# Optimization experiments

Hardware: AMD Instinct MI355X
Metric: run time of the kernel (lower is better)

The kernel has to match this reference:

```python
import jax, jax.numpy as jnp
import numpy as np

NUM_HEADS = 16


def setup_inputs() -> dict:
    key = jax.random.key(0)
    k1, k2, k3 = jax.random.split(key, 3)
    B, S, E = 2, 2048, 1024
    hidden_states = jax.random.normal(k1, (B, S, E), dtype=jnp.float32)
    c_attn_w = jax.random.normal(k2, (E, 3 * E), dtype=jnp.float32) * 0.02
    c_attn_b = jnp.zeros((3 * E,), dtype=jnp.float32)
    c_proj_w = jax.random.normal(k3, (E, E), dtype=jnp.float32) * 0.02
    c_proj_b = jnp.zeros((E,), dtype=jnp.float32)
    return {
        "hidden_states": hidden_states,
        "c_attn_w": c_attn_w,
        "c_attn_b": c_attn_b,
        "c_proj_w": c_proj_w,
        "c_proj_b": c_proj_b,
    }


def reference(hidden_states, c_attn_w, c_attn_b, c_proj_w, c_proj_b):
    B, S, E = hidden_states.shape
    H = NUM_HEADS
    D = E // H
    # Conv1D: qkv projection -> [B, S, 3E]
    qkv = jnp.einsum("bse,ef->bsf", hidden_states, c_attn_w) + c_attn_b
    q, k, v = jnp.split(qkv, 3, axis=-1)
    # split heads -> [B, H, S, D]
    def heads(x):
        return x.reshape(B, S, H, D).transpose(0, 2, 1, 3)
    q, k, v = heads(q), heads(k), heads(v)
    # scaled QK^T -> [B, H, S, S]
    scale = jnp.asarray(D, dtype=q.dtype) ** 0.5
    attn_weights = jnp.einsum("bhqd,bhkd->bhqk", q, k) / scale
    # causal mask (bias buffer): True on/below diagonal
    causal = jnp.tril(jnp.ones((S, S), dtype=bool))
    mask_value = jnp.finfo(attn_weights.dtype).min
    attn_weights = jnp.where(causal[None, None, :, :], attn_weights, mask_value)
    attn_weights = jax.nn.softmax(attn_weights, axis=-1)
    # attn @ V -> merge heads -> [B, S, E]
    attn_out = jnp.einsum("bhqk,bhkd->bhqd", attn_weights, v)
    attn_out = attn_out.transpose(0, 2, 1, 3).reshape(B, S, E)
    # output projection (Conv1D)
    out = jnp.einsum("bse,ef->bsf", attn_out, c_proj_w) + c_proj_b
    return out
```

## Files before the change

kernel.cpp:

```cpp
#include <hip/hip_runtime.h>
#include <stdint.h>

typedef __attribute__((ext_vector_type(8))) __bf16 bf16x8;
typedef __attribute__((ext_vector_type(4))) __bf16 bf16x4;
typedef __attribute__((ext_vector_type(4))) float f32x4;

#define MFMA16(a, b, c) __builtin_amdgcn_mfma_f32_16x16x32_bf16(a, b, c, 0, 0, 0)

__global__ __launch_bounds__(256) void k_cast_bf16(const float* __restrict__ in,
                                                   __bf16* __restrict__ out, int n) {
    int i = (blockIdx.x * 256 + threadIdx.x) * 4;
    if (i >= n) return;
    float4 v = *(const float4*)(in + i);
    bf16x4 o;
    o.x = (__bf16)v.x; o.y = (__bf16)v.y; o.z = (__bf16)v.z; o.w = (__bf16)v.w;
    *(bf16x4*)(out + i) = o;
}

__global__ __launch_bounds__(256) void k_transpose_cast(const float* __restrict__ in,
                                                        __bf16* __restrict__ out,
                                                        int R, int C) {
    __shared__ __bf16 tile[32][33];
    int c0 = blockIdx.x * 32, r0 = blockIdx.y * 32;
    int tx = threadIdx.x, ty = threadIdx.y;
#pragma unroll
    for (int i = 0; i < 4; i++)
        tile[ty + i * 8][tx] = (__bf16)in[(size_t)(r0 + ty + i * 8) * C + c0 + tx];
    __syncthreads();
#pragma unroll
    for (int i = 0; i < 4; i++)
        out[(size_t)(c0 + ty + i * 8) * R + r0 + tx] = tile[tx][ty + i * 8];
}

__global__ __launch_bounds__(256, 2) void k_gemm_qkv(
    const __bf16* __restrict__ A, const __bf16* __restrict__ Bt,
    const float* __restrict__ bias,
    __bf16* __restrict__ Qo, __bf16* __restrict__ Ko, __bf16* __restrict__ Vo) {
    __shared__ __bf16 As[128 * 40];
    __shared__ __bf16 Bs[128 * 40];
    const int Kd = 1024;
    int n0 = blockIdx.x * 128, m0 = blockIdx.y * 128;
    int tid = threadIdx.x;
    int wv = tid >> 6, lane = tid & 63;
    int wm = (wv >> 1) * 64, wn = (wv & 1) * 64;
    int quad = lane >> 4, l16 = lane & 15;
    f32x4 acc[4][4] = {};
    for (int k0 = 0; k0 < Kd; k0 += 32) {
        __syncthreads();
#pragma unroll
        for (int it = 0; it < 2; it++) {
            int c = tid + it * 256;
            int row = c >> 2, kc = (c & 3) << 3;
            *(uint4*)(&As[row * 40 + kc]) = *(const uint4*)(&A[(size_t)(m0 + row) * Kd + k0 + kc]);
            *(uint4*)(&Bs[row * 40 + kc]) = *(const uint4*)(&Bt[(size_t)(n0 + row) * Kd + k0 + kc]);
        }
        __syncthreads();
        bf16x8 af[4], bfr[4];
#pragma unroll
        for (int i = 0; i < 4; i++)
            af[i] = *(const bf16x8*)(&As[(wm + i * 16 + l16) * 40 + quad * 8]);
#pragma unroll
        for (int j = 0; j < 4; j++)
            bfr[j] = *(const bf16x8*)(&Bs[(wn + j * 16 + l16) * 40 + quad * 8]);
#pragma unroll
        for (int i = 0; i < 4; i++)
#pragma unroll
            for (int j = 0; j < 4; j++)
                acc[i][j] = MFMA16(af[i], bfr[j], acc[i][j]);
    }
#pragma unroll
    for (int i = 0; i < 4; i++) {
#pragma unroll
        for (int j = 0; j < 4; j++) {
            int n = n0 + wn + j * 16 + l16;
            float bv = bias[n];
            int sec = n >> 10, nl = n & 1023;
            int h = nl >> 6, d = nl & 63;
            int mbase = m0 + wm + i * 16 + quad * 4;
            int bb = mbase >> 11, s = mbase & 2047;
            if (sec == 2) {
                bf16x4 v4;
#pragma unroll
                for (int r = 0; r < 4; r++) v4[r] = (__bf16)(acc[i][j][r] + bv);
                *(bf16x4*)(&Vo[((size_t)(bb * 16 + h) * 64 + d) * 2048 + s]) = v4;
            } else {
                __bf16* dst = sec == 0 ? Qo : Ko;
                float scl = (sec == 0) ? 0.125f : 1.0f;
#pragma unroll
                for (int r = 0; r < 4; r++)
                    dst[((size_t)(bb * 16 + h) * 2048 + (s + r)) * 64 + d] =
                        (__bf16)((acc[i][j][r] + bv) * scl);
            }
        }
    }
}

__global__ __launch_bounds__(256, 2) void k_gemm_proj(
    const __bf16* __restrict__ A, const __bf16* __restrict__ Bt,
    const float* __restrict__ bias, float* __restrict__ out) {
    __shared__ __bf16 As[128 * 40];
    __shared__ __bf16 Bs[128 * 40];
    const int Kd = 1024;
    int n0 = blockIdx.x * 128, m0 = blockIdx.y * 128;
    int tid = threadIdx.x;
    int wv = tid >> 6, lane = tid & 63;
    int wm = (wv >> 1) * 64, wn = (wv & 1) * 64;
    int quad = lane >> 4, l16 = lane & 15;
    f32x4 acc[4][4] = {};
    for (int k0 = 0; k0 < Kd; k0 += 32) {
        __syncthreads();
#pragma unroll
        for (int it = 0; it < 2; it++) {
            int c = tid + it * 256;
            int row = c >> 2, kc = (c & 3) << 3;
            *(uint4*)(&As[row * 40 + kc]) = *(const uint4*)(&A[(size_t)(m0 + row) * Kd + k0 + kc]);
            *(uint4*)(&Bs[row * 40 + kc]) = *(const uint4*)(&Bt[(size_t)(n0 + row) * Kd + k0 + kc]);
        }
        __syncthreads();
        bf16x8 af[4], bfr[4];
#pragma unroll
        for (int i = 0; i < 4; i++)
            af[i] = *(const bf16x8*)(&As[(wm + i * 16 + l16) * 40 + quad * 8]);
#pragma unroll
        for (int j = 0; j < 4; j++)
            bfr[j] = *(const bf16x8*)(&Bs[(wn + j * 16 + l16) * 40 + quad * 8]);
#pragma unroll
        for (int i = 0; i < 4; i++)
#pragma unroll
            for (int j = 0; j < 4; j++)
                acc[i][j] = MFMA16(af[i], bfr[j], acc[i][j]);
    }
#pragma unroll
    for (int i = 0; i < 4; i++) {
#pragma unroll
        for (int j = 0; j < 4; j++) {
            int n = n0 + wn + j * 16 + l16;
            float bv = bias[n];
#pragma unroll
            for (int r = 0; r < 4; r++) {
                int m = m0 + wm + i * 16 + quad * 4 + r;
                out[(size_t)m * 1024 + n] = acc[i][j][r] + bv;
            }
        }
    }
}

__global__ __launch_bounds__(256, 2) void k_attn(
    const __bf16* __restrict__ Qg, const __bf16* __restrict__ Kg,
    const __bf16* __restrict__ Vtg, __bf16* __restrict__ Og) {
    __shared__ __bf16 Ks[64 * 72];
    __shared__ __bf16 Vt[64 * 72];
    __shared__ __bf16 Ps[64 * 72];
    int bh = blockIdx.x >> 4;
    int tp = blockIdx.x & 15;
    int b = bh >> 4, h = bh & 15;
    const __bf16* Qp = Qg + (size_t)bh * 2048 * 64;
    const __bf16* Kp = Kg + (size_t)bh * 2048 * 64;
    const __bf16* Vp = Vtg + (size_t)bh * 64 * 2048;
    int tid = threadIdx.x, wv = tid >> 6, lane = tid & 63;
    int quad = lane >> 4, l16 = lane & 15;
    int tt0 = tp, tt1 = 31 - tp;

    bf16x8 qf[2][2];
#pragma unroll
    for (int ks = 0; ks < 2; ks++) {
        qf[0][ks] = *(const bf16x8*)(&Qp[(size_t)(tt0 * 64 + wv * 16 + l16) * 64 + ks * 32 + quad * 8]);
        qf[1][ks] = *(const bf16x8*)(&Qp[(size_t)(tt1 * 64 + wv * 16 + l16) * 64 + ks * 32 + quad * 8]);
    }
    float m_i[2] = {-1e30f, -1e30f}, l_i[2] = {0.f, 0.f};
    f32x4 acc_o[2][4] = {};

    int nkt = tt1 + 1;
    for (int kt = 0; kt < nkt; kt++) {
        __syncthreads();
#pragma unroll
        for (int it = 0; it < 2; it++) {
            int idx = tid * 2 + it;
            int row = idx >> 3, cc = (idx & 7) * 8;
            *(uint4*)(&Ks[row * 72 + cc]) =
                *(const uint4*)(&Kp[(size_t)(kt * 64 + row) * 64 + cc]);
            *(uint4*)(&Vt[row * 72 + cc]) =
                *(const uint4*)(&Vp[(size_t)row * 2048 + kt * 64 + cc]);
        }
        __syncthreads();
        bf16x8 kf[4][2], vf[4][2];
#pragma unroll
        for (int i = 0; i < 4; i++)
#pragma unroll
            for (int ks = 0; ks < 2; ks++) {
                kf[i][ks] = *(const bf16x8*)(&Ks[(i * 16 + l16) * 72 + ks * 32 + quad * 8]);
                vf[i][ks] = *(const bf16x8*)(&Vt[(i * 16 + l16) * 72 + ks * 32 + quad * 8]);
            }
#pragma unroll
        for (int tt = 0; tt < 2; tt++) {
            int t = tt ? tt1 : tt0;
            if (kt > t) continue;
            f32x4 s[4] = {};
#pragma unroll
            for (int ks = 0; ks < 2; ks++)
#pragma unroll
                for (int i = 0; i < 4; i++) s[i] = MFMA16(kf[i][ks], qf[tt][ks], s[i]);
            if (kt == t) {
                int ql = wv * 16 + l16;
#pragma unroll
                for (int i = 0; i < 4; i++)
#pragma unroll
                    for (int r = 0; r < 4; r++)
                        if (i * 16 + quad * 4 + r > ql) s[i][r] = -1e30f;
            }
            float mx = s[0][0];
#pragma unroll
            for (int i = 0; i < 4; i++)
#pragma unroll
                for (int r = 0; r < 4; r++) mx = fmaxf(mx, s[i][r]);
            mx = fmaxf(mx, __shfl_xor(mx, 16));
            mx = fmaxf(mx, __shfl_xor(mx, 32));
            float mnew = fmaxf(m_i[tt], mx);
            float al = __expf(m_i[tt] - mnew);
            m_i[tt] = mnew;
            float rs = 0.f;
#pragma unroll
            for (int i = 0; i < 4; i++) {
                bf16x4 pk;
#pragma unroll
                for (int r = 0; r < 4; r++) {
                    float p = __expf(s[i][r] - mnew);
                    rs += p;
                    pk[r] = (__bf16)p;
                }
                *(bf16x4*)(&Ps[(wv * 16 + l16) * 72 + i * 16 + quad * 4]) = pk;
            }
            rs += __shfl_xor(rs, 16);
            rs += __shfl_xor(rs, 32);
            l_i[tt] = l_i[tt] * al + rs;
#pragma unroll
            for (int i = 0; i < 4; i++)
#pragma unroll
                for (int r = 0; r < 4; r++) acc_o[tt][i][r] *= al;
#pragma unroll
            for (int ks = 0; ks < 2; ks++) {
                bf16x8 pf = *(const bf16x8*)(&Ps[(wv * 16 + l16) * 72 + ks * 32 + quad * 8]);
#pragma unroll
                for (int i = 0; i < 4; i++) acc_o[tt][i] = MFMA16(vf[i][ks], pf, acc_o[tt][i]);
            }
        }
    }
#pragma unroll
    for (int tt = 0; tt < 2; tt++) {
        int t = tt ? tt1 : tt0;
        int q = t * 64 + wv * 16 + l16;
        float inv = 1.f / l_i[tt];
#pragma unroll
        for (int i = 0; i < 4; i++) {
            bf16x4 o4;
#pragma unroll
            for (int r = 0; r < 4; r++) o4[r] = (__bf16)(acc_o[tt][i][r] * inv);
            *(bf16x4*)(&Og[((size_t)b * 2048 + q) * 1024 + h * 64 + i * 16 + quad * 4]) = o4;
        }
    }
}

extern "C" void kernel_launch(void* const* d_in, const int* in_sizes, int n_in,
                              void* d_out, int out_size, void* d_ws, size_t ws_size,
                              hipStream_t stream) {
    const float* hs = (const float*)d_in[0];
    const float* w1 = (const float*)d_in[1];
    const float* b1 = (const float*)d_in[2];
    const float* w2 = (const float*)d_in[3];
    const float* b2 = (const float*)d_in[4];
    float* out = (float*)d_out;

    char* ws = (char*)d_ws;
    __bf16* hsb = (__bf16*)(ws);
    __bf16* w1t = (__bf16*)(ws + (size_t)8 * 1024 * 1024);
    __bf16* w2t = (__bf16*)(ws + (size_t)14 * 1024 * 1024);
    __bf16* Qb  = (__bf16*)(ws + (size_t)16 * 1024 * 1024);
    __bf16* Kb  = (__bf16*)(ws + (size_t)24 * 1024 * 1024);
    __bf16* Vb  = (__bf16*)(ws + (size_t)32 * 1024 * 1024);
    __bf16* AOb = (__bf16*)(ws + (size_t)40 * 1024 * 1024);

    k_cast_bf16<<<4096, 256, 0, stream>>>(hs, hsb, 4096 * 1024);
    k_transpose_cast<<<dim3(96, 32), dim3(32, 8), 0, stream>>>(w1, w1t, 1024, 3072);
    k_transpose_cast<<<dim3(32, 32), dim3(32, 8), 0, stream>>>(w2, w2t, 1024, 1024);
    k_gemm_qkv<<<dim3(24, 32), 256, 0, stream>>>(hsb, w1t, b1, Qb, Kb, Vb);
    k_attn<<<512, 256, 0, stream>>>(Qb, Kb, Vb, AOb);
    k_gemm_proj<<<dim3(8, 32), 256, 0, stream>>>(AOb, w2t, b2, out);
}
```

Measured before the change: 199.5 us.

## Use direct global-to-LDS loads in GEMMs and one query tile per attention block

Both GEMM kernels now load A and B tiles with global_load_lds, which writes directly into unpadded LDS. This skips the register staging round trip but drops the bank-conflict padding. The attention kernel drops the paired-tile scheme and processes one query tile per block, launching twice as many blocks with heaviest tiles scheduled first. That lowers per-block register state and improves parallelism, at the cost of possible load imbalance and more K/V reloads.

```diff
diff --git a/kernel.cpp b/kernel.cpp
--- a/kernel.cpp
+++ b/kernel.cpp
@@ -6,6 +6,12 @@
 typedef __attribute__((ext_vector_type(4))) float f32x4;
 
 #define MFMA16(a, b, c) __builtin_amdgcn_mfma_f32_16x16x32_bf16(a, b, c, 0, 0, 0)
+
+__device__ __forceinline__ void async_ld16(const __bf16* g, __bf16* lds_base) {
+    __builtin_amdgcn_global_load_lds(
+        (const __attribute__((address_space(1))) void*)g,
+        (__attribute__((address_space(3))) void*)lds_base, 16, 0, 0);
+}
 
 __global__ __launch_bounds__(256) void k_cast_bf16(const float* __restrict__ in,
                                                    __bf16* __restrict__ out, int n) {
@@ -36,32 +42,32 @@
     const __bf16* __restrict__ A, const __bf16* __restrict__ Bt,
     const float* __restrict__ bias,
     __bf16* __restrict__ Qo, __bf16* __restrict__ Ko, __bf16* __restrict__ Vo) {
-    __shared__ __bf16 As[128 * 40];
-    __shared__ __bf16 Bs[128 * 40];
+    __shared__ __bf16 As[128 * 32];
+    __shared__ __bf16 Bs[128 * 32];
     const int Kd = 1024;
     int n0 = blockIdx.x * 128, m0 = blockIdx.y * 128;
     int tid = threadIdx.x;
     int wv = tid >> 6, lane = tid & 63;
     int wm = (wv >> 1) * 64, wn = (wv & 1) * 64;
     int quad = lane >> 4, l16 = lane & 15;
+    int lrow = lane >> 2, lcol = (lane & 3) * 8;
     f32x4 acc[4][4] = {};
     for (int k0 = 0; k0 < Kd; k0 += 32) {
         __syncthreads();
 #pragma unroll
-        for (int it = 0; it < 2; it++) {
-            int c = tid + it * 256;
-            int row = c >> 2, kc = (c & 3) << 3;
-            *(uint4*)(&As[row * 40 + kc]) = *(const uint4*)(&A[(size_t)(m0 + row) * Kd + k0 + kc]);
-            *(uint4*)(&Bs[row * 40 + kc]) = *(const uint4*)(&Bt[(size_t)(n0 + row) * Kd + k0 + kc]);
+        for (int r = 0; r < 2; r++) {
+            int row = r * 64 + wv * 16;
+            async_ld16(&A[(size_t)(m0 + row + lrow) * Kd + k0 + lcol], &As[row * 32]);
+            async_ld16(&Bt[(size_t)(n0 + row + lrow) * Kd + k0 + lcol], &Bs[row * 32]);
         }
         __syncthreads();
         bf16x8 af[4], bfr[4];
 #pragma unroll
         for (int i = 0; i < 4; i++)
-            af[i] = *(const bf16x8*)(&As[(wm + i * 16 + l16) * 40 + quad * 8]);
+            af[i] = *(const bf16x8*)(&As[(wm + i * 16 + l16) * 32 + quad * 8]);
 #pragma unroll
         for (int j = 0; j < 4; j++)
-            bfr[j] = *(const bf16x8*)(&Bs[(wn + j * 16 + l16) * 40 + quad * 8]);
+            bfr[j] = *(const bf16x8*)(&Bs[(wn + j * 16 + l16) * 32 + quad * 8]);
 #pragma unroll
         for (int i = 0; i < 4; i++)
 #pragma unroll
@@ -98,32 +104,32 @@
 __global__ __launch_bounds__(256, 2) void k_gemm_proj(
     const __bf16* __restrict__ A, const __bf16* __restrict__ Bt,
     const float* __restrict__ bias, float* __restrict__ out) {
-    __shared__ __bf16 As[128 * 40];
-    __shared__ __bf16 Bs[128 * 40];
+    __shared__ __bf16 As[128 * 32];
+    __shared__ __bf16 Bs[128 * 32];
     const int Kd = 1024;
     int n0 = blockIdx.x * 128, m0 = blockIdx.y * 128;
     int tid = threadIdx.x;
     int wv = tid >> 6, lane = tid & 63;
     int wm = (wv >> 1) * 64, wn = (wv & 1) * 64;
     int quad = lane >> 4, l16 = lane & 15;
+    int lrow = lane >> 2, lcol = (lane & 3) * 8;
     f32x4 acc[4][4] = {};
     for (int k0 = 0; k0 < Kd; k0 += 32) {
         __syncthreads();
 #pragma unroll
-        for (int it = 0; it < 2; it++) {
-            int c = tid + it * 256;
-            int row = c >> 2, kc = (c & 3) << 3;
-            *(uint4*)(&As[row * 40 + kc]) = *(const uint4*)(&A[(size_t)(m0 + row) * Kd + k0 + kc]);
-            *(uint4*)(&Bs[row * 40 + kc]) = *(const uint4*)(&Bt[(size_t)(n0 + row) * Kd + k0 + kc]);
+        for (int r = 0; r < 2; r++) {
+            int row = r * 64 + wv * 16;
+            async_ld16(&A[(size_t)(m0 + row + lrow) * Kd + k0 + lcol], &As[row * 32]);
+            async_ld16(&Bt[(size_t)(n0 + row + lrow) * Kd + k0 + lcol], &Bs[row * 32]);
         }
         __syncthreads();
         bf16x8 af[4], bfr[4];
 #pragma unroll
         for (int i = 0; i < 4; i++)
-            af[i] = *(const bf16x8*)(&As[(wm + i * 16 + l16) * 40 + quad * 8]);
+            af[i] = *(const bf16x8*)(&As[(wm + i * 16 + l16) * 32 + quad * 8]);
 #pragma unroll
         for (int j = 0; j < 4; j++)
-            bfr[j] = *(const bf16x8*)(&Bs[(wn + j * 16 + l16) * 40 + quad * 8]);
+            bfr[j] = *(const bf16x8*)(&Bs[(wn + j * 16 + l16) * 32 + quad * 8]);
 #pragma unroll
         for (int i = 0; i < 4; i++)
 #pragma unroll
@@ -151,27 +157,23 @@
     __shared__ __bf16 Ks[64 * 72];
     __shared__ __bf16 Vt[64 * 72];
     __shared__ __bf16 Ps[64 * 72];
-    int bh = blockIdx.x >> 4;
-    int tp = blockIdx.x & 15;
+    int bh = blockIdx.x & 31;
+    int t = 31 - (blockIdx.x >> 5);
     int b = bh >> 4, h = bh & 15;
     const __bf16* Qp = Qg + (size_t)bh * 2048 * 64;
     const __bf16* Kp = Kg + (size_t)bh * 2048 * 64;
     const __bf16* Vp = Vtg + (size_t)bh * 64 * 2048;
     int tid = threadIdx.x, wv = tid >> 6, lane = tid & 63;
     int quad = lane >> 4, l16 = lane & 15;
-    int tt0 = tp, tt1 = 31 - tp;
-
-    bf16x8 qf[2][2];
-#pragma unroll
-    for (int ks = 0; ks < 2; ks++) {
-        qf[0][ks] = *(const bf16x8*)(&Qp[(size_t)(tt0 * 64 + wv * 16 + l16) * 64 + ks * 32 + quad * 8]);
-        qf[1][ks] = *(const bf16x8*)(&Qp[(size_t)(tt1 * 64 + wv * 16 + l16) * 64 + ks * 32 + quad * 8]);
-    }
-    float m_i[2] = {-1e30f, -1e30f}, l_i[2] = {0.f, 0.f};
-    f32x4 acc_o[2][4] = {};
-
-    int nkt = tt1 + 1;
-    for (int kt = 0; kt < nkt; kt++) {
+
+    bf16x8 qf[2];
+#pragma unroll
+    for (int ks = 0; ks < 2; ks++)
+        qf[ks] = *(const bf16x8*)(&Qp[(size_t)(t * 64 + wv * 16 + l16) * 64 + ks * 32 + quad * 8]);
+    float m_i = -1e30f, l_i = 0.f;
+    f32x4 acc_o[4] = {};
+
+    for (int kt = 0; kt <= t; kt++) {
         __syncthreads();
 #pragma unroll
         for (int it = 0; it < 2; it++) {
@@ -191,72 +193,63 @@
                 kf[i][ks] = *(const bf16x8*)(&Ks[(i * 16 + l16) * 72 + ks * 32 + quad * 8]);
                 vf[i][ks] = *(const bf16x8*)(&Vt[(i * 16 + l16) * 72 + ks * 32 + quad * 8]);
             }
-#pragma unroll
-        for (int tt = 0; tt < 2; tt++) {
-            int t = tt ? tt1 : tt0;
-            if (kt > t) continue;
-            f32x4 s[4] = {};
-#pragma unroll
-            for (int ks = 0; ks < 2; ks++)
-#pragma unroll
-                for (int i = 0; i < 4; i++) s[i] = MFMA16(kf[i][ks], qf[tt][ks], s[i]);
-            if (kt == t) {
-                int ql = wv * 16 + l16;
-#pragma unroll
-                for (int i = 0; i < 4; i++)
-#pragma unroll
-                    for (int r = 0; r < 4; r++)
-                        if (i * 16 + quad * 4 + r > ql) s[i][r] = -1e30f;
-            }
-            float mx = s[0][0];
+        f32x4 s[4] = {};
+#pragma unroll
+        for (int ks = 0; ks < 2; ks++)
+#pragma unroll
+            for (int i = 0; i < 4; i++) s[i] = MFMA16(kf[i][ks], qf[ks], s[i]);
+        if (kt == t) {
+            int ql = wv * 16 + l16;
 #pragma unroll
             for (int i = 0; i < 4; i++)
 #pragma unroll
-                for (int r = 0; r < 4; r++) mx = fmaxf(mx, s[i][r]);
-            mx = fmaxf(mx, __shfl_xor(mx, 16));
-            mx = fmaxf(mx, __shfl_xor(mx, 32));
-            float mnew = fmaxf(m_i[tt], mx);
-            float al = __expf(m_i[tt] - mnew);
-            m_i[tt] = mnew;
-            float rs = 0.f;
-#pragma unroll
-            for (int i = 0; i < 4; i++) {
-                bf16x4 pk;
-#pragma unroll
-                for (int r = 0; r < 4; r++) {
-                    float p = __expf(s[i][r] - mnew);
-                    rs += p;
-                    pk[r] = (__bf16)p;
-                }
-                *(bf16x4*)(&Ps[(wv * 16 + l16) * 72 + i * 16 + quad * 4]) = pk;
-            }
-            rs += __shfl_xor(rs, 16);
-            rs += __shfl_xor(rs, 32);
-            l_i[tt] = l_i[tt] * al + rs;
-#pragma unroll
-            for (int i = 0; i < 4; i++)
-#pragma unroll
-                for (int r = 0; r < 4; r++) acc_o[tt][i][r] *= al;
-#pragma unroll
-            for (int ks = 0; ks < 2; ks++) {
-                bf16x8 pf = *(const bf16x8*)(&Ps[(wv * 16 + l16) * 72 + ks * 32 + quad * 8]);
-#pragma unroll
-                for (int i = 0; i < 4; i++) acc_o[tt][i] = MFMA16(vf[i][ks], pf, acc_o[tt][i]);
-            }
-        }
-    }
-#pragma unroll
-    for (int tt = 0; tt < 2; tt++) {
-        int t = tt ? tt1 : tt0;
-        int q = t * 64 + wv * 16 + l16;
-        float inv = 1.f / l_i[tt];
+                for (int r = 0; r < 4; r++)
+                    if (i * 16 + quad * 4 + r > ql) s[i][r] = -1e30f;
+        }
+        float mx = s[0][0];
+#pragma unroll
+        for (int i = 0; i < 4; i++)
+#pragma unroll
+            for (int r = 0; r < 4; r++) mx = fmaxf(mx, s[i][r]);
+        mx = fmaxf(mx, __shfl_xor(mx, 16));
+        mx = fmaxf(mx, __shfl_xor(mx, 32));
+        float mnew = fmaxf(m_i, mx);
+        float al = __expf(m_i - mnew);
+        m_i = mnew;
+        float rs = 0.f;
 #pragma unroll
         for (int i = 0; i < 4; i++) {
-            bf16x4 o4;
-#pragma unroll
-            for (int r = 0; r < 4; r++) o4[r] = (__bf16)(acc_o[tt][i][r] * inv);
-            *(bf16x4*)(&Og[((size_t)b * 2048 + q) * 1024 + h * 64 + i * 16 + quad * 4]) = o4;
-        }
+            bf16x4 pk;
+#pragma unroll
+            for (int r = 0; r < 4; r++) {
+                float p = __expf(s[i][r] - mnew);
+                rs += p;
+                pk[r] = (__bf16)p;
+            }
+            *(bf16x4*)(&Ps[(wv * 16 + l16) * 72 + i * 16 + quad * 4]) = pk;
+        }
+        rs += __shfl_xor(rs, 16);
+        rs += __shfl_xor(rs, 32);
+        l_i = l_i * al + rs;
+#pragma unroll
+        for (int i = 0; i < 4; i++)
+#pragma unroll
+            for (int r = 0; r < 4; r++) acc_o[i][r] *= al;
+#pragma unroll
+        for (int ks = 0; ks < 2; ks++) {
+            bf16x8 pf = *(const bf16x8*)(&Ps[(wv * 16 + l16) * 72 + ks * 32 + quad * 8]);
+#pragma unroll
+            for (int i = 0; i < 4; i++) acc_o[i] = MFMA16(vf[i][ks], pf, acc_o[i]);
+        }
+    }
+    int q = t * 64 + wv * 16 + l16;
+    float inv = 1.f / l_i;
+#pragma unroll
+    for (int i = 0; i < 4; i++) {
+        bf16x4 o4;
+#pragma unroll
+        for (int r = 0; r < 4; r++) o4[r] = (__bf16)(acc_o[i][r] * inv);
+        *(bf16x4*)(&Og[((size_t)b * 2048 + q) * 1024 + h * 64 + i * 16 + quad * 4]) = o4;
     }
 }
 
@@ -283,6 +276,6 @@
     k_transpose_cast<<<dim3(96, 32), dim3(32, 8), 0, stream>>>(w1, w1t, 1024, 3072);
     k_transpose_cast<<<dim3(32, 32), dim3(32, 8), 0, stream>>>(w2, w2t, 1024, 1024);
     k_gemm_qkv<<<dim3(24, 32), 256, 0, stream>>>(hsb, w1t, b1, Qb, Kb, Vb);
-    k_attn<<<512, 256, 0, stream>>>(Qb, Kb, Vb, AOb);
+    k_attn<<<1024, 256, 0, stream>>>(Qb, Kb, Vb, AOb);
     k_gemm_proj<<<dim3(8, 32), 256, 0, stream>>>(AOb, w2t, b2, out);
 }
```

Result: faster. 189.0 us (-5.3%).
